# Kernel tuning notes

Hardware: AMD Instinct MI355X
Metric: run time of the kernel (lower is better)

Reference implementation:

```python
import jax, jax.numpy as jnp
import numpy as np

N_NODES = 40000
IN_CH, HID_CH, OUT_CH = 128, 128, 64
N_EDGES = 640000
N_LABEL = 200000


def gcn_conv(x, edge_index, W, b):
    """PyG-style GCNConv: x' = D^{-1/2}(A+I)D^{-1/2} (x W) + b."""
    n = x.shape[0]
    loops = jnp.arange(n, dtype=edge_index.dtype)
    src = jnp.concatenate([edge_index[0], loops])  # [E+N]
    dst = jnp.concatenate([edge_index[1], loops])  # [E+N]
    deg = jax.ops.segment_sum(jnp.ones_like(dst, dtype=x.dtype), dst, num_segments=n)
    dinv = jnp.where(deg > 0, jax.lax.rsqrt(deg), 0.0)
    norm = dinv[src] * dinv[dst]                   # [E+N]
    h = x @ W                                      # [n, out]
    msg = h[src] * norm[:, None]                   # gather + scale
    agg = jax.ops.segment_sum(msg, dst, num_segments=n)
    return agg + b


def setup_inputs() -> dict:
    key = jax.random.key(0)
    k = jax.random.split(key, 8)
    x = jax.random.normal(k[0], (N_NODES, IN_CH), dtype=jnp.float32)
    edge_index = jax.random.randint(k[1], (2, N_EDGES), 0, N_NODES, dtype=jnp.int64)
    edge_label_index = jax.random.randint(k[2], (2, N_LABEL), 0, N_NODES, dtype=jnp.int64)
    s1 = 1.0 / np.sqrt(IN_CH)
    s2 = 1.0 / np.sqrt(HID_CH)
    W1 = jax.random.uniform(k[3], (IN_CH, HID_CH), jnp.float32, -s1, s1)
    b1 = jnp.zeros((HID_CH,), jnp.float32)
    W2 = jax.random.uniform(k[4], (HID_CH, OUT_CH), jnp.float32, -s2, s2)
    b2 = jnp.zeros((OUT_CH,), jnp.float32)
    return {"x": x, "edge_index": edge_index, "edge_label_index": edge_label_index,
            "W1": W1, "b1": b1, "W2": W2, "b2": b2}


def reference(x, edge_index, edge_label_index, W1, b1, W2, b2):
    # encode: conv1 -> relu -> conv2
    h = jax.nn.relu(gcn_conv(x, edge_index, W1, b1))
    z = gcn_conv(h, edge_index, W2, b2)            # [N, OUT_CH]
    # decode: dot-product score per candidate edge
    logits = jnp.sum(z[edge_label_index[0]] * z[edge_label_index[1]], axis=-1)
    return logits
```

## Files before the change

kernel.cpp:

```cpp
#include <hip/hip_runtime.h>
#include <hip/hip_bf16.h>

constexpr int IN_CH  = 128;
constexpr int HID_CH = 128;
constexpr int OUT_CH = 64;
constexpr int SCAN_CHUNK = 1024;

typedef __attribute__((ext_vector_type(8))) short bf16x8;
typedef __attribute__((ext_vector_type(4))) float f32x4;


__device__ inline unsigned short f2bf(float f) {
  __hip_bfloat16 h = __float2bfloat16(f);
  return *reinterpret_cast<unsigned short*>(&h);
}
__device__ inline unsigned pack_bf16x2(float lo, float hi) {
  return (unsigned)f2bf(lo) | ((unsigned)f2bf(hi) << 16);
}
__device__ inline float bf_lo(unsigned u) { return __uint_as_float(u << 16); }
__device__ inline float bf_hi(unsigned u) { return __uint_as_float(u & 0xffff0000u); }


__global__ __launch_bounds__(256) void k_zero(int* __restrict__ a, int n) {
  int i = (blockIdx.x * 256 + threadIdx.x) * 4;
  if (i + 3 < n) *(int4*)&a[i] = make_int4(0, 0, 0, 0);
  else for (int j = 0; j < 4 && i + j < n; ++j) a[i + j] = 0;
}


__global__ void k_count(const int* __restrict__ dst, int* __restrict__ cnt,
                        int* __restrict__ ord, int E) {
  int e = (blockIdx.x * blockDim.x + threadIdx.x) * 4;
  if (e + 3 < E) {
    int4 v = *(const int4*)&dst[e];
    int4 o;
    o.x = atomicAdd(&cnt[v.x], 1);
    o.y = atomicAdd(&cnt[v.y], 1);
    o.z = atomicAdd(&cnt[v.z], 1);
    o.w = atomicAdd(&cnt[v.w], 1);
    *(int4*)&ord[e] = o;
  } else {
    for (int j = 0; j < 4 && e + j < E; ++j) ord[e + j] = atomicAdd(&cnt[dst[e + j]], 1);
  }
}

__global__ __launch_bounds__(256) void k_scan_part(const int* __restrict__ cnt,
                                                   int* __restrict__ bsum,
                                                   float* __restrict__ dinv, int N) {
  int t = threadIdx.x;
  int base = blockIdx.x * SCAN_CHUNK + t * 4;
  int s = 0;
  if (base + 3 < N) {
    int4 v = *(const int4*)&cnt[base];
    s = v.x + v.y + v.z + v.w;
    float4 d;
    d.x = rsqrtf((float)v.x + 1.0f);
    d.y = rsqrtf((float)v.y + 1.0f);
    d.z = rsqrtf((float)v.z + 1.0f);
    d.w = rsqrtf((float)v.w + 1.0f);
    *(float4*)&dinv[base] = d;
  } else {
    for (int j = 0; j < 4; ++j)
      if (base + j < N) {
        int c = cnt[base + j];
        s += c;
        dinv[base + j] = rsqrtf((float)c + 1.0f);
      }
  }
  __shared__ int red[256];
  red[t] = s; __syncthreads();
  for (int off = 128; off; off >>= 1) {
    if (t < off) red[t] += red[t + off];
    __syncthreads();
  }
  if (t == 0) bsum[blockIdx.x] = red[0];
}

__global__ __launch_bounds__(256) void k_scan_fill(const int* __restrict__ cnt,
                                                   const int* __restrict__ bsum,
                                                   int* __restrict__ rowptr, int N, int E) {
  int t = threadIdx.x;
  int boff = 0;
  for (int i = 0; i < blockIdx.x; ++i) boff += bsum[i];
  int base = blockIdx.x * SCAN_CHUNK + t * 4;
  int v[4] = {0, 0, 0, 0};
  if (base + 3 < N) {
    int4 q = *(const int4*)&cnt[base];
    v[0] = q.x; v[1] = q.y; v[2] = q.z; v[3] = q.w;
  } else {
    for (int j = 0; j < 4; ++j) if (base + j < N) v[j] = cnt[base + j];
  }
  int mysum = v[0] + v[1] + v[2] + v[3];
  __shared__ int s[256];
  s[t] = mysum; __syncthreads();
  for (int off = 1; off < 256; off <<= 1) {
    int add = (t >= off) ? s[t - off] : 0;
    __syncthreads();
    s[t] += add;
    __syncthreads();
  }
  int run = boff + s[t] - mysum;
  for (int j = 0; j < 4; ++j) {
    if (base + j < N) rowptr[base + j] = run;
    run += v[j];
  }
  if (blockIdx.x == 0 && t == 0) rowptr[N] = E;
}

__global__ void k_fill(const int* __restrict__ src, const int* __restrict__ dst,
                       const int* __restrict__ ord, const int* __restrict__ rowptr,
                       int* __restrict__ col, int E) {
  int e0 = (blockIdx.x * blockDim.x + threadIdx.x) * 4;
  if (e0 >= E) return;
  if (e0 + 3 < E) {
    int4 sv = *(const int4*)&src[e0];
    int4 dv = *(const int4*)&dst[e0];
    int4 ov = *(const int4*)&ord[e0];
    col[rowptr[dv.x] + ov.x] = sv.x;
    col[rowptr[dv.y] + ov.y] = sv.y;
    col[rowptr[dv.z] + ov.z] = sv.z;
    col[rowptr[dv.w] + ov.w] = sv.w;
  } else {
    for (int j = 0; j < 4 && e0 + j < E; ++j)
      col[rowptr[dst[e0 + j]] + ord[e0 + j]] = src[e0 + j];
  }
}


template <int OUT, bool A_BF16>
__global__ __launch_bounds__(256) void k_gemm(const void* __restrict__ Xv,
                                              const float* __restrict__ W,
                                              const float* __restrict__ dinv,
                                              unsigned short* __restrict__ Y, int N) {
  constexpr int KD = 128;
  __shared__ unsigned short Wt[OUT * KD];
  int t = threadIdx.x;
  for (int i = t * 4; i < KD * OUT; i += 1024) {
    int k = i / OUT, c = i % OUT;
    float4 w4 = *(const float4*)&W[i];
    float wa[4] = {w4.x, w4.y, w4.z, w4.w};
#pragma unroll
    for (int j = 0; j < 4; ++j) {
      int colj = c + j;
      int byte = colj * (KD * 2) + k * 2;
      byte ^= ((colj & 7) << 4);
      *(unsigned short*)((char*)Wt + byte) = f2bf(wa[j]);
    }
  }
  __syncthreads();

  int w = t >> 6, l = t & 63;
  int lr = l & 15, kg = (l >> 4) * 8;
  int r = blockIdx.x * 64 + w * 16 + lr;
  bool valid = r < N;

  f32x4 acc[OUT / 16];
#pragma unroll
  for (int n = 0; n < OUT / 16; ++n) acc[n] = f32x4{0.f, 0.f, 0.f, 0.f};

#pragma unroll
  for (int kb = 0; kb < KD / 32; ++kb) {
    bf16x8 a = bf16x8{0, 0, 0, 0, 0, 0, 0, 0};
    if (valid) {
      if (A_BF16) {
        a = *(const bf16x8*)((const unsigned short*)Xv + (size_t)r * KD + kb * 32 + kg);
      } else {
        const float* xrow = (const float*)Xv + (size_t)r * KD + kb * 32 + kg;
        float4 x0 = *(const float4*)xrow;
        float4 x1 = *(const float4*)(xrow + 4);
        a[0] = (short)f2bf(x0.x); a[1] = (short)f2bf(x0.y);
        a[2] = (short)f2bf(x0.z); a[3] = (short)f2bf(x0.w);
        a[4] = (short)f2bf(x1.x); a[5] = (short)f2bf(x1.y);
        a[6] = (short)f2bf(x1.z); a[7] = (short)f2bf(x1.w);
      }
    }
#pragma unroll
    for (int n = 0; n < OUT / 16; ++n) {
      int col = n * 16 + lr;
      int byte = col * (KD * 2) + (kb * 32 + kg) * 2;
      byte ^= ((col & 7) << 4);
      bf16x8 b = *(const bf16x8*)((const char*)Wt + byte);
      acc[n] = __builtin_amdgcn_mfma_f32_16x16x32_bf16(a, b, acc[n], 0, 0, 0);
    }
  }

  int orow = blockIdx.x * 64 + w * 16 + (l >> 4) * 4;
  float dn[4];
#pragma unroll
  for (int i = 0; i < 4; ++i) dn[i] = (orow + i < N) ? dinv[orow + i] : 0.f;
#pragma unroll
  for (int i = 0; i < 4; ++i) {
    if (orow + i >= N) continue;
#pragma unroll
    for (int n = 0; n < OUT / 16; ++n)
      Y[(size_t)(orow + i) * OUT + n * 16 + lr] = f2bf(acc[n][i] * dn[i]);
  }
}


__global__ __launch_bounds__(256) void k_agg128(const unsigned* __restrict__ HS,
                                                const int* __restrict__ rowptr,
                                                const int* __restrict__ col,
                                                const float* __restrict__ dinv,
                                                const float* __restrict__ bias,
                                                unsigned* __restrict__ Outb, int N) {
  int n = blockIdx.x * 4 + (threadIdx.x >> 6);
  if (n >= N) return;
  int l = threadIdx.x & 63;
  float dn = dinv[n];
  unsigned u0 = HS[(size_t)n * 64 + l];
  float ax = bf_lo(u0), ay = bf_hi(u0);
  int p = rowptr[n], pend = rowptr[n + 1];
  for (; p + 8 <= pend; p += 8) {
    int s[8]; unsigned g[8];
#pragma unroll
    for (int j = 0; j < 8; ++j) s[j] = col[p + j];
#pragma unroll
    for (int j = 0; j < 8; ++j) g[j] = HS[(size_t)s[j] * 64 + l];
#pragma unroll
    for (int j = 0; j < 8; ++j) { ax += bf_lo(g[j]); ay += bf_hi(g[j]); }
  }
  for (; p < pend; ++p) {
    unsigned g = HS[(size_t)col[p] * 64 + l];
    ax += bf_lo(g); ay += bf_hi(g);
  }
  float2 b2 = ((const float2*)bias)[l];
  Outb[(size_t)n * 64 + l] =
      pack_bf16x2(fmaxf(dn * ax + b2.x, 0.f), fmaxf(dn * ay + b2.y, 0.f));
}


__global__ __launch_bounds__(256) void k_agg64(const unsigned* __restrict__ HS,
                                               const int* __restrict__ rowptr,
                                               const int* __restrict__ col,
                                               const float* __restrict__ dinv,
                                               const float* __restrict__ bias,
                                               unsigned* __restrict__ Zu, int N) {
  int n = blockIdx.x * 8 + (threadIdx.x >> 5);
  if (n >= N) return;
  int g = threadIdx.x & 31;
  float dn = dinv[n];
  unsigned u0 = HS[(size_t)n * 32 + g];
  float ax = bf_lo(u0), ay = bf_hi(u0);
  int p = rowptr[n], pend = rowptr[n + 1];
  for (; p + 8 <= pend; p += 8) {
    int s[8]; unsigned q[8];
#pragma unroll
    for (int j = 0; j < 8; ++j) s[j] = col[p + j];
#pragma unroll
    for (int j = 0; j < 8; ++j) q[j] = HS[(size_t)s[j] * 32 + g];
#pragma unroll
    for (int j = 0; j < 8; ++j) { ax += bf_lo(q[j]); ay += bf_hi(q[j]); }
  }
  for (; p < pend; ++p) {
    unsigned q = HS[(size_t)col[p] * 32 + g];
    ax += bf_lo(q); ay += bf_hi(q);
  }
  float2 b2 = ((const float2*)bias)[g];
  Zu[(size_t)n * 32 + g] = pack_bf16x2(dn * ax + b2.x, dn * ay + b2.y);
}


__global__ __launch_bounds__(256) void k_decode(const uint4* __restrict__ Z,
                                                const int* __restrict__ ia,
                                                const int* __restrict__ ib,
                                                float* __restrict__ out, int L) {
  int t = blockIdx.x * 256 + threadIdx.x;
  int i = t >> 3;
  if (i >= L) return;
  int e = t & 7;
  int a = ia[i], b = ib[i];
  uint4 za = Z[(size_t)a * 8 + e];
  uint4 zb = Z[(size_t)b * 8 + e];
  float p = bf_lo(za.x) * bf_lo(zb.x) + bf_hi(za.x) * bf_hi(zb.x)
          + bf_lo(za.y) * bf_lo(zb.y) + bf_hi(za.y) * bf_hi(zb.y)
          + bf_lo(za.z) * bf_lo(zb.z) + bf_hi(za.z) * bf_hi(zb.z)
          + bf_lo(za.w) * bf_lo(zb.w) + bf_hi(za.w) * bf_hi(zb.w);
  p += __shfl_xor(p, 1);
  p += __shfl_xor(p, 2);
  p += __shfl_xor(p, 4);
  if (e == 0) out[i] = p;
}

extern "C" void kernel_launch(void* const* d_in, const int* in_sizes, int n_in,
                              void* d_out, int out_size, void* d_ws, size_t ws_size,
                              hipStream_t stream) {
  const float* x   = (const float*)d_in[0];
  const int*   ei  = (const int*)d_in[1];
  const int*   eli = (const int*)d_in[2];
  const float* W1  = (const float*)d_in[3];
  const float* b1  = (const float*)d_in[4];
  const float* W2  = (const float*)d_in[5];
  const float* b2  = (const float*)d_in[6];
  float* logits = (float*)d_out;

  int N = in_sizes[0] / IN_CH;
  int E = in_sizes[1] / 2;
  int L = in_sizes[2] / 2;
  const int* src = ei;
  const int* dst = ei + E;
  const int* la  = eli;
  const int* lb  = eli + L;

  char* ws = (char*)d_ws;
  size_t off = 0;
  auto alloc = [&](size_t bytes) {
    void* p = ws + off;
    off = (off + bytes + 255) & ~(size_t)255;
    return p;
  };
  int*      cnt    = (int*)alloc((size_t)N * 4);
  int*      rowptr = (int*)alloc((size_t)(N + 1) * 4);
  float*    dinv   = (float*)alloc((size_t)N * 4);
  int*      col    = (int*)alloc((size_t)E * 4);
  int*      ord    = (int*)alloc((size_t)E * 4);
  unsigned short* hs  = (unsigned short*)alloc((size_t)N * HID_CH * 2);
  unsigned* hrb    = (unsigned*)alloc((size_t)N * HID_CH * 2);
  unsigned short* h2s = (unsigned short*)alloc((size_t)N * OUT_CH * 2);
  unsigned* zu     = (unsigned*)alloc((size_t)N * OUT_CH * 2);
  int*      bsum   = (int*)alloc(256 * 4);

  const int TB = 256;
  int nscan = (N + SCAN_CHUNK - 1) / SCAN_CHUNK;
  k_zero<<<(N / 4 + TB - 1) / TB, TB, 0, stream>>>(cnt, N);
  k_count<<<(E / 4 + TB - 1) / TB, TB, 0, stream>>>(dst, cnt, ord, E);
  k_scan_part<<<nscan, 256, 0, stream>>>(cnt, bsum, dinv, N);
  k_scan_fill<<<nscan, 256, 0, stream>>>(cnt, bsum, rowptr, N, E);
  k_fill <<<(E / 4 + TB - 1) / TB, TB, 0, stream>>>(src, dst, ord, rowptr, col, E);

  k_gemm<HID_CH, false><<<(N + 63) / 64, 256, 0, stream>>>(x, W1, dinv, hs, N);
  k_agg128<<<(N + 3) / 4, 256, 0, stream>>>((const unsigned*)hs, rowptr, col, dinv, b1, hrb, N);

  k_gemm<OUT_CH, true><<<(N + 63) / 64, 256, 0, stream>>>(hrb, W2, dinv, h2s, N);
  k_agg64<<<(N + 7) / 8, 256, 0, stream>>>((const unsigned*)h2s, rowptr, col, dinv, b2, zu, N);

  k_decode<<<((size_t)L * 8 + 255) / 256, 256, 0, stream>>>((const uint4*)zu, la, lb, logits, L);
}
```

Baseline: 135.3 us.

## Split feature tables into 32-channel planes mapped to XCDs for L2 locality

Stores hidden and output features as planar 32-channel slices (pass-major) instead of row-major, and assigns each slice to a fixed subset of XCDs via block-id decoding so each XCD's L2 only caches its slice during gathers. Aggregation now uses 16-lane groups with four edge streams per node reduced by shuffles, replacing separate agg128/agg64 kernels with one template. Decode is split across two planes with atomicAdd into a zeroed output, which adds a zeroing step and atomics and relies on the block-to-XCD round-robin assumption.

After: 213.2 us. 57.6% more time.

```diff
diff --git a/kernel.cpp b/kernel.cpp
--- a/kernel.cpp
+++ b/kernel.cpp
@@ -21,10 +21,13 @@
 __device__ inline float bf_hi(unsigned u) { return __uint_as_float(u & 0xffff0000u); }
 
 
-__global__ __launch_bounds__(256) void k_zero(int* __restrict__ a, int n) {
+__global__ __launch_bounds__(256) void k_zero(int* __restrict__ a, int na,
+                                              float* __restrict__ b, int nb) {
   int i = (blockIdx.x * 256 + threadIdx.x) * 4;
-  if (i + 3 < n) *(int4*)&a[i] = make_int4(0, 0, 0, 0);
-  else for (int j = 0; j < 4 && i + j < n; ++j) a[i + j] = 0;
+  if (i + 3 < na) *(int4*)&a[i] = make_int4(0, 0, 0, 0);
+  else for (int j = 0; j < 4 && i + j < na; ++j) a[i + j] = 0;
+  if (i + 3 < nb) *(float4*)&b[i] = make_float4(0.f, 0.f, 0.f, 0.f);
+  else for (int j = 0; j < 4 && i + j < nb; ++j) b[i + j] = 0.f;
 }
 
 
@@ -163,7 +166,7 @@
     bf16x8 a = bf16x8{0, 0, 0, 0, 0, 0, 0, 0};
     if (valid) {
       if (A_BF16) {
-        a = *(const bf16x8*)((const unsigned short*)Xv + (size_t)r * KD + kb * 32 + kg);
+        a = *(const bf16x8*)((const unsigned short*)Xv + ((size_t)kb * N + r) * 32 + kg);
       } else {
         const float* xrow = (const float*)Xv + (size_t)r * KD + kb * 32 + kg;
         float4 x0 = *(const float4*)xrow;
@@ -193,93 +196,85 @@
     if (orow + i >= N) continue;
 #pragma unroll
     for (int n = 0; n < OUT / 16; ++n)
-      Y[(size_t)(orow + i) * OUT + n * 16 + lr] = f2bf(acc[n][i] * dn[i]);
-  }
-}
-
-
-__global__ __launch_bounds__(256) void k_agg128(const unsigned* __restrict__ HS,
-                                                const int* __restrict__ rowptr,
-                                                const int* __restrict__ col,
-                                                const float* __restrict__ dinv,
-                                                const float* __restrict__ bias,
-                                                unsigned* __restrict__ Outb, int N) {
-  int n = blockIdx.x * 4 + (threadIdx.x >> 6);
+      Y[((size_t)(n >> 1) * N + (orow + i)) * 32 + (n & 1) * 16 + lr] =
+          f2bf(acc[n][i] * dn[i]);
+  }
+}
+
+
+template <int NPASS, bool RELU>
+__global__ __launch_bounds__(256) void k_agg(const unsigned* __restrict__ T,
+                                             const int* __restrict__ rowptr,
+                                             const int* __restrict__ col,
+                                             const float* __restrict__ dinv,
+                                             const float* __restrict__ bias,
+                                             unsigned* __restrict__ Out, int N) {
+  constexpr int SUBS = 8 / NPASS;
+  int bid = blockIdx.x;
+  int xcd = bid & 7, chunk = bid >> 3;
+  int pass = xcd / SUBS, sub = xcd % SUBS;
+  int w = threadIdx.x >> 6, l = threadIdx.x & 63;
+  int n = (chunk * SUBS + sub) * 4 + w;
   if (n >= N) return;
-  int l = threadIdx.x & 63;
+  int grp = l >> 4, cp = l & 15;
+  const unsigned* Tp = T + (size_t)pass * N * 16;
   float dn = dinv[n];
-  unsigned u0 = HS[(size_t)n * 64 + l];
-  float ax = bf_lo(u0), ay = bf_hi(u0);
-  int p = rowptr[n], pend = rowptr[n + 1];
-  for (; p + 8 <= pend; p += 8) {
-    int s[8]; unsigned g[8];
-#pragma unroll
-    for (int j = 0; j < 8; ++j) s[j] = col[p + j];
-#pragma unroll
-    for (int j = 0; j < 8; ++j) g[j] = HS[(size_t)s[j] * 64 + l];
-#pragma unroll
-    for (int j = 0; j < 8; ++j) { ax += bf_lo(g[j]); ay += bf_hi(g[j]); }
-  }
-  for (; p < pend; ++p) {
-    unsigned g = HS[(size_t)col[p] * 64 + l];
-    ax += bf_lo(g); ay += bf_hi(g);
-  }
-  float2 b2 = ((const float2*)bias)[l];
-  Outb[(size_t)n * 64 + l] =
-      pack_bf16x2(fmaxf(dn * ax + b2.x, 0.f), fmaxf(dn * ay + b2.y, 0.f));
-}
-
-
-__global__ __launch_bounds__(256) void k_agg64(const unsigned* __restrict__ HS,
-                                               const int* __restrict__ rowptr,
-                                               const int* __restrict__ col,
-                                               const float* __restrict__ dinv,
-                                               const float* __restrict__ bias,
-                                               unsigned* __restrict__ Zu, int N) {
-  int n = blockIdx.x * 8 + (threadIdx.x >> 5);
-  if (n >= N) return;
-  int g = threadIdx.x & 31;
-  float dn = dinv[n];
-  unsigned u0 = HS[(size_t)n * 32 + g];
-  float ax = bf_lo(u0), ay = bf_hi(u0);
-  int p = rowptr[n], pend = rowptr[n + 1];
-  for (; p + 8 <= pend; p += 8) {
-    int s[8]; unsigned q[8];
-#pragma unroll
-    for (int j = 0; j < 8; ++j) s[j] = col[p + j];
-#pragma unroll
-    for (int j = 0; j < 8; ++j) q[j] = HS[(size_t)s[j] * 32 + g];
-#pragma unroll
-    for (int j = 0; j < 8; ++j) { ax += bf_lo(q[j]); ay += bf_hi(q[j]); }
-  }
-  for (; p < pend; ++p) {
-    unsigned q = HS[(size_t)col[p] * 32 + g];
-    ax += bf_lo(q); ay += bf_hi(q);
-  }
-  float2 b2 = ((const float2*)bias)[g];
-  Zu[(size_t)n * 32 + g] = pack_bf16x2(dn * ax + b2.x, dn * ay + b2.y);
-}
-
-
-__global__ __launch_bounds__(256) void k_decode(const uint4* __restrict__ Z,
+  float ax = 0.f, ay = 0.f;
+  if (grp == 0) {
+    unsigned u0 = Tp[(size_t)n * 16 + cp];
+    ax = bf_lo(u0); ay = bf_hi(u0);
+  }
+  int pend = rowptr[n + 1];
+  int e = rowptr[n] + grp;
+  for (; e + 12 < pend; e += 16) {
+    int c0 = __builtin_nontemporal_load(&col[e]);
+    int c1 = __builtin_nontemporal_load(&col[e + 4]);
+    int c2 = __builtin_nontemporal_load(&col[e + 8]);
+    int c3 = __builtin_nontemporal_load(&col[e + 12]);
+    unsigned u0 = Tp[(size_t)c0 * 16 + cp];
+    unsigned u1 = Tp[(size_t)c1 * 16 + cp];
+    unsigned u2 = Tp[(size_t)c2 * 16 + cp];
+    unsigned u3 = Tp[(size_t)c3 * 16 + cp];
+    ax += bf_lo(u0) + bf_lo(u1) + bf_lo(u2) + bf_lo(u3);
+    ay += bf_hi(u0) + bf_hi(u1) + bf_hi(u2) + bf_hi(u3);
+  }
+  for (; e < pend; e += 4) {
+    int c = __builtin_nontemporal_load(&col[e]);
+    unsigned u = Tp[(size_t)c * 16 + cp];
+    ax += bf_lo(u); ay += bf_hi(u);
+  }
+  ax += __shfl_xor(ax, 16); ax += __shfl_xor(ax, 32);
+  ay += __shfl_xor(ay, 16); ay += __shfl_xor(ay, 32);
+  if (grp == 0) {
+    float2 b2 = ((const float2*)(bias + pass * 32))[cp];
+    float vx = dn * ax + b2.x, vy = dn * ay + b2.y;
+    if (RELU) { vx = fmaxf(vx, 0.f); vy = fmaxf(vy, 0.f); }
+    Out[(size_t)pass * N * 16 + (size_t)n * 16 + cp] = pack_bf16x2(vx, vy);
+  }
+}
+
+
+__global__ __launch_bounds__(256) void k_decode(const unsigned* __restrict__ Z,
                                                 const int* __restrict__ ia,
                                                 const int* __restrict__ ib,
-                                                float* __restrict__ out, int L) {
-  int t = blockIdx.x * 256 + threadIdx.x;
-  int i = t >> 3;
+                                                float* __restrict__ out, int N, int L) {
+  int bid = blockIdx.x;
+  int xcd = bid & 7, chunk = bid >> 3;
+  int pass = xcd >> 2, sub = xcd & 3;
+  int t = threadIdx.x;
+  int i = (chunk * 4 + sub) * 16 + (t >> 4);
   if (i >= L) return;
-  int e = t & 7;
+  int e = t & 15;
   int a = ia[i], b = ib[i];
-  uint4 za = Z[(size_t)a * 8 + e];
-  uint4 zb = Z[(size_t)b * 8 + e];
-  float p = bf_lo(za.x) * bf_lo(zb.x) + bf_hi(za.x) * bf_hi(zb.x)
-          + bf_lo(za.y) * bf_lo(zb.y) + bf_hi(za.y) * bf_hi(zb.y)
-          + bf_lo(za.z) * bf_lo(zb.z) + bf_hi(za.z) * bf_hi(zb.z)
-          + bf_lo(za.w) * bf_lo(zb.w) + bf_hi(za.w) * bf_hi(zb.w);
+  const unsigned* Zp = Z + (size_t)pass * N * 16;
+  unsigned za = Zp[(size_t)a * 16 + e];
+  unsigned zb = Zp[(size_t)b * 16 + e];
+  float p = bf_lo(za) * bf_lo(zb) + bf_hi(za) * bf_hi(zb);
   p += __shfl_xor(p, 1);
   p += __shfl_xor(p, 2);
   p += __shfl_xor(p, 4);
-  if (e == 0) out[i] = p;
+  p += __shfl_xor(p, 8);
+  if (e == 0) atomicAdd(&out[i], p);
 }
 
 extern "C" void kernel_launch(void* const* d_in, const int* in_sizes, int n_in,
@@ -314,25 +309,29 @@
   float*    dinv   = (float*)alloc((size_t)N * 4);
   int*      col    = (int*)alloc((size_t)E * 4);
   int*      ord    = (int*)alloc((size_t)E * 4);
-  unsigned short* hs  = (unsigned short*)alloc((size_t)N * HID_CH * 2);
-  unsigned* hrb    = (unsigned*)alloc((size_t)N * HID_CH * 2);
-  unsigned short* h2s = (unsigned short*)alloc((size_t)N * OUT_CH * 2);
-  unsigned* zu     = (unsigned*)alloc((size_t)N * OUT_CH * 2);
+  unsigned short* hsp  = (unsigned short*)alloc((size_t)N * HID_CH * 2);
+  unsigned short* hrbp = (unsigned short*)alloc((size_t)N * HID_CH * 2);
+  unsigned short* h2sp = (unsigned short*)alloc((size_t)N * OUT_CH * 2);
+  unsigned short* zup  = (unsigned short*)alloc((size_t)N * OUT_CH * 2);
   int*      bsum   = (int*)alloc(256 * 4);
 
   const int TB = 256;
   int nscan = (N + SCAN_CHUNK - 1) / SCAN_CHUNK;
-  k_zero<<<(N / 4 + TB - 1) / TB, TB, 0, stream>>>(cnt, N);
+  int nzero = max(N, L);
+  k_zero<<<(nzero / 4 + TB - 1) / TB, TB, 0, stream>>>(cnt, N, logits, L);
   k_count<<<(E / 4 + TB - 1) / TB, TB, 0, stream>>>(dst, cnt, ord, E);
   k_scan_part<<<nscan, 256, 0, stream>>>(cnt, bsum, dinv, N);
   k_scan_fill<<<nscan, 256, 0, stream>>>(cnt, bsum, rowptr, N, E);
   k_fill <<<(E / 4 + TB - 1) / TB, TB, 0, stream>>>(src, dst, ord, rowptr, col, E);
 
-  k_gemm<HID_CH, false><<<(N + 63) / 64, 256, 0, stream>>>(x, W1, dinv, hs, N);
-  k_agg128<<<(N + 3) / 4, 256, 0, stream>>>((const unsigned*)hs, rowptr, col, dinv, b1, hrb, N);
-
-  k_gemm<OUT_CH, true><<<(N + 63) / 64, 256, 0, stream>>>(hrb, W2, dinv, h2s, N);
-  k_agg64<<<(N + 7) / 8, 256, 0, stream>>>((const unsigned*)h2s, rowptr, col, dinv, b2, zu, N);
-
-  k_decode<<<((size_t)L * 8 + 255) / 256, 256, 0, stream>>>((const uint4*)zu, la, lb, logits, L);
-}
+  k_gemm<HID_CH, false><<<(N + 63) / 64, 256, 0, stream>>>(x, W1, dinv, hsp, N);
+  k_agg<4, true><<<((N + 7) / 8) * 8, 256, 0, stream>>>(
+      (const unsigned*)hsp, rowptr, col, dinv, b1, (unsigned*)hrbp, N);
+
+  k_gemm<OUT_CH, true><<<(N + 63) / 64, 256, 0, stream>>>(hrbp, W2, dinv, h2sp, N);
+  k_agg<2, false><<<((N + 15) / 16) * 8, 256, 0, stream>>>(
+      (const unsigned*)h2sp, rowptr, col, dinv, b2, (unsigned*)zup, N);
+
+  k_decode<<<((L + 63) / 64) * 8, 256, 0, stream>>>(
+      (const unsigned*)zup, la, lb, logits, N, L);
+}
```

## Split feature tables into two column halves with XCD-aware aggregation scheduling

Applied to the files above, without the earlier changes.

The GEMM outputs and aggregation outputs now use a two-plane layout, each plane holding half the feature columns for all nodes. The aggregation kernel is unified into a template and maps block IDs so blocks on XCDs 0-3 handle the first half and XCDs 4-7 the second. The aim is to shrink each XCD's gather working set so it stays in its L2. It also adds nontemporal loads of the column indices and a 4-edge tail step, at the cost of more complex indexing in the GEMM, aggregation and decode kernels.

After: 144.4 us. +6.7%, slower.

```diff
diff --git a/kernel.cpp b/kernel.cpp
--- a/kernel.cpp
+++ b/kernel.cpp
@@ -133,6 +133,7 @@
                                               const float* __restrict__ dinv,
                                               unsigned short* __restrict__ Y, int N) {
   constexpr int KD = 128;
+  constexpr int NCG = OUT / 32;
   __shared__ unsigned short Wt[OUT * KD];
   int t = threadIdx.x;
   for (int i = t * 4; i < KD * OUT; i += 1024) {
@@ -163,7 +164,8 @@
     bf16x8 a = bf16x8{0, 0, 0, 0, 0, 0, 0, 0};
     if (valid) {
       if (A_BF16) {
-        a = *(const bf16x8*)((const unsigned short*)Xv + (size_t)r * KD + kb * 32 + kg);
+        a = *(const bf16x8*)((const unsigned short*)Xv +
+                             ((size_t)(kb >> 1) * N + r) * 64 + (kb & 1) * 32 + kg);
       } else {
         const float* xrow = (const float*)Xv + (size_t)r * KD + kb * 32 + kg;
         float4 x0 = *(const float4*)xrow;
@@ -193,85 +195,75 @@
     if (orow + i >= N) continue;
 #pragma unroll
     for (int n = 0; n < OUT / 16; ++n)
-      Y[(size_t)(orow + i) * OUT + n * 16 + lr] = f2bf(acc[n][i] * dn[i]);
-  }
-}
-
-
-__global__ __launch_bounds__(256) void k_agg128(const unsigned* __restrict__ HS,
-                                                const int* __restrict__ rowptr,
-                                                const int* __restrict__ col,
-                                                const float* __restrict__ dinv,
-                                                const float* __restrict__ bias,
-                                                unsigned* __restrict__ Outb, int N) {
-  int n = blockIdx.x * 4 + (threadIdx.x >> 6);
+      Y[((size_t)(n / NCG) * N + (orow + i)) * (OUT / 2) + (n % NCG) * 16 + lr] =
+          f2bf(acc[n][i] * dn[i]);
+  }
+}
+
+
+template <int CPU, bool RELU>
+__global__ __launch_bounds__(256) void k_agg(const unsigned* __restrict__ T,
+                                             const int* __restrict__ rowptr,
+                                             const int* __restrict__ col,
+                                             const float* __restrict__ dinv,
+                                             const float* __restrict__ bias,
+                                             unsigned* __restrict__ Out, int N) {
+  constexpr int NPW = 64 / CPU;
+  constexpr int NPB = 4 * NPW;
+  int bid = blockIdx.x;
+  int xcd = bid & 7, chunk = bid >> 3;
+  int pass = xcd >> 2, sub = xcd & 3;
+  int w = threadIdx.x >> 6, l = threadIdx.x & 63;
+  int n = (chunk * 4 + sub) * NPB + w * NPW + l / CPU;
   if (n >= N) return;
-  int l = threadIdx.x & 63;
+  int cp = l % CPU;
+  const unsigned* Tp = T + (size_t)pass * N * CPU;
   float dn = dinv[n];
-  unsigned u0 = HS[(size_t)n * 64 + l];
+  unsigned u0 = Tp[(size_t)n * CPU + cp];
   float ax = bf_lo(u0), ay = bf_hi(u0);
   int p = rowptr[n], pend = rowptr[n + 1];
   for (; p + 8 <= pend; p += 8) {
     int s[8]; unsigned g[8];
 #pragma unroll
-    for (int j = 0; j < 8; ++j) s[j] = col[p + j];
-#pragma unroll
-    for (int j = 0; j < 8; ++j) g[j] = HS[(size_t)s[j] * 64 + l];
+    for (int j = 0; j < 8; ++j) s[j] = __builtin_nontemporal_load(&col[p + j]);
+#pragma unroll
+    for (int j = 0; j < 8; ++j) g[j] = Tp[(size_t)s[j] * CPU + cp];
 #pragma unroll
     for (int j = 0; j < 8; ++j) { ax += bf_lo(g[j]); ay += bf_hi(g[j]); }
   }
+  if (p + 4 <= pend) {
+    int s[4]; unsigned g[4];
+#pragma unroll
+    for (int j = 0; j < 4; ++j) s[j] = __builtin_nontemporal_load(&col[p + j]);
+#pragma unroll
+    for (int j = 0; j < 4; ++j) g[j] = Tp[(size_t)s[j] * CPU + cp];
+#pragma unroll
+    for (int j = 0; j < 4; ++j) { ax += bf_lo(g[j]); ay += bf_hi(g[j]); }
+    p += 4;
+  }
   for (; p < pend; ++p) {
-    unsigned g = HS[(size_t)col[p] * 64 + l];
+    unsigned g = Tp[(size_t)__builtin_nontemporal_load(&col[p]) * CPU + cp];
     ax += bf_lo(g); ay += bf_hi(g);
   }
-  float2 b2 = ((const float2*)bias)[l];
-  Outb[(size_t)n * 64 + l] =
-      pack_bf16x2(fmaxf(dn * ax + b2.x, 0.f), fmaxf(dn * ay + b2.y, 0.f));
-}
-
-
-__global__ __launch_bounds__(256) void k_agg64(const unsigned* __restrict__ HS,
-                                               const int* __restrict__ rowptr,
-                                               const int* __restrict__ col,
-                                               const float* __restrict__ dinv,
-                                               const float* __restrict__ bias,
-                                               unsigned* __restrict__ Zu, int N) {
-  int n = blockIdx.x * 8 + (threadIdx.x >> 5);
-  if (n >= N) return;
-  int g = threadIdx.x & 31;
-  float dn = dinv[n];
-  unsigned u0 = HS[(size_t)n * 32 + g];
-  float ax = bf_lo(u0), ay = bf_hi(u0);
-  int p = rowptr[n], pend = rowptr[n + 1];
-  for (; p + 8 <= pend; p += 8) {
-    int s[8]; unsigned q[8];
-#pragma unroll
-    for (int j = 0; j < 8; ++j) s[j] = col[p + j];
-#pragma unroll
-    for (int j = 0; j < 8; ++j) q[j] = HS[(size_t)s[j] * 32 + g];
-#pragma unroll
-    for (int j = 0; j < 8; ++j) { ax += bf_lo(q[j]); ay += bf_hi(q[j]); }
-  }
-  for (; p < pend; ++p) {
-    unsigned q = HS[(size_t)col[p] * 32 + g];
-    ax += bf_lo(q); ay += bf_hi(q);
-  }
-  float2 b2 = ((const float2*)bias)[g];
-  Zu[(size_t)n * 32 + g] = pack_bf16x2(dn * ax + b2.x, dn * ay + b2.y);
-}
-
-
-__global__ __launch_bounds__(256) void k_decode(const uint4* __restrict__ Z,
+  float2 b2 = ((const float2*)bias)[pass * CPU + cp];
+  float vx = dn * ax + b2.x, vy = dn * ay + b2.y;
+  if (RELU) { vx = fmaxf(vx, 0.f); vy = fmaxf(vy, 0.f); }
+  Out[(size_t)pass * N * CPU + (size_t)n * CPU + cp] = pack_bf16x2(vx, vy);
+}
+
+
+__global__ __launch_bounds__(256) void k_decode(const unsigned* __restrict__ Z,
                                                 const int* __restrict__ ia,
                                                 const int* __restrict__ ib,
-                                                float* __restrict__ out, int L) {
+                                                float* __restrict__ out, int N, int L) {
   int t = blockIdx.x * 256 + threadIdx.x;
   int i = t >> 3;
   if (i >= L) return;
   int e = t & 7;
   int a = ia[i], b = ib[i];
-  uint4 za = Z[(size_t)a * 8 + e];
-  uint4 zb = Z[(size_t)b * 8 + e];
+  size_t base = (size_t)(e >> 2) * N * 16 + (size_t)(e & 3) * 4;
+  uint4 za = *(const uint4*)&Z[base + (size_t)a * 16];
+  uint4 zb = *(const uint4*)&Z[base + (size_t)b * 16];
   float p = bf_lo(za.x) * bf_lo(zb.x) + bf_hi(za.x) * bf_hi(zb.x)
           + bf_lo(za.y) * bf_lo(zb.y) + bf_hi(za.y) * bf_hi(zb.y)
           + bf_lo(za.z) * bf_lo(zb.z) + bf_hi(za.z) * bf_hi(zb.z)
@@ -314,10 +306,10 @@
   float*    dinv   = (float*)alloc((size_t)N * 4);
   int*      col    = (int*)alloc((size_t)E * 4);
   int*      ord    = (int*)alloc((size_t)E * 4);
-  unsigned short* hs  = (unsigned short*)alloc((size_t)N * HID_CH * 2);
-  unsigned* hrb    = (unsigned*)alloc((size_t)N * HID_CH * 2);
-  unsigned short* h2s = (unsigned short*)alloc((size_t)N * OUT_CH * 2);
-  unsigned* zu     = (unsigned*)alloc((size_t)N * OUT_CH * 2);
+  unsigned short* hsp  = (unsigned short*)alloc((size_t)N * HID_CH * 2);
+  unsigned short* hrbp = (unsigned short*)alloc((size_t)N * HID_CH * 2);
+  unsigned short* h2sp = (unsigned short*)alloc((size_t)N * OUT_CH * 2);
+  unsigned short* zup  = (unsigned short*)alloc((size_t)N * OUT_CH * 2);
   int*      bsum   = (int*)alloc(256 * 4);
 
   const int TB = 256;
@@ -328,11 +320,20 @@
   k_scan_fill<<<nscan, 256, 0, stream>>>(cnt, bsum, rowptr, N, E);
   k_fill <<<(E / 4 + TB - 1) / TB, TB, 0, stream>>>(src, dst, ord, rowptr, col, E);
 
-  k_gemm<HID_CH, false><<<(N + 63) / 64, 256, 0, stream>>>(x, W1, dinv, hs, N);
-  k_agg128<<<(N + 3) / 4, 256, 0, stream>>>((const unsigned*)hs, rowptr, col, dinv, b1, hrb, N);
-
-  k_gemm<OUT_CH, true><<<(N + 63) / 64, 256, 0, stream>>>(hrb, W2, dinv, h2s, N);
-  k_agg64<<<(N + 7) / 8, 256, 0, stream>>>((const unsigned*)h2s, rowptr, col, dinv, b2, zu, N);
-
-  k_decode<<<((size_t)L * 8 + 255) / 256, 256, 0, stream>>>((const uint4*)zu, la, lb, logits, L);
-}
+  k_gemm<HID_CH, false><<<(N + 63) / 64, 256, 0, stream>>>(x, W1, dinv, hsp, N);
+  {
+    int nchunk = (N + 8 * 4 - 1) / (8 * 4);
+    k_agg<32, true><<<nchunk * 8, 256, 0, stream>>>(
+        (const unsigned*)hsp, rowptr, col, dinv, b1, (unsigned*)hrbp, N);
+  }
+
+  k_gemm<OUT_CH, true><<<(N + 63) / 64, 256, 0, stream>>>(hrbp, W2, dinv, h2sp, N);
+  {
+    int nchunk = (N + 16 * 4 - 1) / (16 * 4);
+    k_agg<16, false><<<nchunk * 8, 256, 0, stream>>>(
+        (const unsigned*)h2sp, rowptr, col, dinv, b2, (unsigned*)zup, N);
+  }
+
+  k_decode<<<((size_t)L * 8 + 255) / 256, 256, 0, stream>>>(
+      (const unsigned*)zup, la, lb, logits, N, L);
+}
```

## Merge scan kernels, fuse CSR fill with first GEMM, widen aggregation loads

Applied to the files above, without the earlier changes.

Replaces the two-pass prefix scan with a single kernel that chains block partials through flags and spin-waits on earlier blocks, and zeroes those flags in the existing zero kernel. The CSR column fill and the first GEMM now share one launch, split by block index. Both aggregation kernels move to 8-byte loads per lane with half as many lanes per node, add a 4-wide tail step, and read column indices with nontemporal loads. The goal is fewer launches and less per-lane gather overhead. The spin-wait relies on all 40 scan blocks being resident at once.

After: 129.2 us, median of 2. 4.5% less time.

```diff
diff --git a/kernel.cpp b/kernel.cpp
--- a/kernel.cpp
+++ b/kernel.cpp
@@ -21,10 +21,13 @@
 __device__ inline float bf_hi(unsigned u) { return __uint_as_float(u & 0xffff0000u); }
 
 
-__global__ __launch_bounds__(256) void k_zero(int* __restrict__ a, int n) {
+__global__ __launch_bounds__(256) void k_zero(int* __restrict__ a, int na,
+                                              int* __restrict__ b, int nb) {
   int i = (blockIdx.x * 256 + threadIdx.x) * 4;
-  if (i + 3 < n) *(int4*)&a[i] = make_int4(0, 0, 0, 0);
-  else for (int j = 0; j < 4 && i + j < n; ++j) a[i + j] = 0;
+  if (i + 3 < na) *(int4*)&a[i] = make_int4(0, 0, 0, 0);
+  else for (int j = 0; j < 4 && i + j < na; ++j) a[i + j] = 0;
+  if (i + 3 < nb) *(int4*)&b[i] = make_int4(0, 0, 0, 0);
+  else for (int j = 0; j < 4 && i + j < nb; ++j) b[i + j] = 0;
 }
 
 
@@ -44,51 +47,30 @@
   }
 }
 
-__global__ __launch_bounds__(256) void k_scan_part(const int* __restrict__ cnt,
-                                                   int* __restrict__ bsum,
-                                                   float* __restrict__ dinv, int N) {
-  int t = threadIdx.x;
-  int base = blockIdx.x * SCAN_CHUNK + t * 4;
-  int s = 0;
+__global__ __launch_bounds__(256) void k_scan_lb(const int* __restrict__ cnt,
+                                                 int* __restrict__ rowptr,
+                                                 float* __restrict__ dinv,
+                                                 int* __restrict__ flags,
+                                                 int* __restrict__ partial,
+                                                 int N, int E) {
+  int t = threadIdx.x, bid = blockIdx.x;
+  int base = bid * SCAN_CHUNK + t * 4;
+  int v[4] = {0, 0, 0, 0};
   if (base + 3 < N) {
-    int4 v = *(const int4*)&cnt[base];
-    s = v.x + v.y + v.z + v.w;
+    int4 q = *(const int4*)&cnt[base];
+    v[0] = q.x; v[1] = q.y; v[2] = q.z; v[3] = q.w;
     float4 d;
-    d.x = rsqrtf((float)v.x + 1.0f);
-    d.y = rsqrtf((float)v.y + 1.0f);
-    d.z = rsqrtf((float)v.z + 1.0f);
-    d.w = rsqrtf((float)v.w + 1.0f);
+    d.x = rsqrtf((float)v[0] + 1.0f);
+    d.y = rsqrtf((float)v[1] + 1.0f);
+    d.z = rsqrtf((float)v[2] + 1.0f);
+    d.w = rsqrtf((float)v[3] + 1.0f);
     *(float4*)&dinv[base] = d;
   } else {
     for (int j = 0; j < 4; ++j)
       if (base + j < N) {
-        int c = cnt[base + j];
-        s += c;
-        dinv[base + j] = rsqrtf((float)c + 1.0f);
+        v[j] = cnt[base + j];
+        dinv[base + j] = rsqrtf((float)v[j] + 1.0f);
       }
-  }
-  __shared__ int red[256];
-  red[t] = s; __syncthreads();
-  for (int off = 128; off; off >>= 1) {
-    if (t < off) red[t] += red[t + off];
-    __syncthreads();
-  }
-  if (t == 0) bsum[blockIdx.x] = red[0];
-}
-
-__global__ __launch_bounds__(256) void k_scan_fill(const int* __restrict__ cnt,
-                                                   const int* __restrict__ bsum,
-                                                   int* __restrict__ rowptr, int N, int E) {
-  int t = threadIdx.x;
-  int boff = 0;
-  for (int i = 0; i < blockIdx.x; ++i) boff += bsum[i];
-  int base = blockIdx.x * SCAN_CHUNK + t * 4;
-  int v[4] = {0, 0, 0, 0};
-  if (base + 3 < N) {
-    int4 q = *(const int4*)&cnt[base];
-    v[0] = q.x; v[1] = q.y; v[2] = q.z; v[3] = q.w;
-  } else {
-    for (int j = 0; j < 4; ++j) if (base + j < N) v[j] = cnt[base + j];
   }
   int mysum = v[0] + v[1] + v[2] + v[3];
   __shared__ int s[256];
@@ -99,39 +81,38 @@
     s[t] += add;
     __syncthreads();
   }
-  int run = boff + s[t] - mysum;
+  if (t == 255) {
+    partial[bid] = s[255];
+    __threadfence();
+    atomicExch(&flags[bid], 1);
+  }
+  int pv = 0;
+  if (t < bid) {
+    while (atomicAdd(&flags[t], 0) == 0) {}
+    __threadfence();
+    pv = atomicAdd(&partial[t], 0);
+  }
+  __shared__ int boff_s;
+  if (t < 64) {
+#pragma unroll
+    for (int off = 32; off; off >>= 1) pv += __shfl_down(pv, off);
+    if (t == 0) boff_s = pv;
+  }
+  __syncthreads();
+  int run = boff_s + s[t] - mysum;
   for (int j = 0; j < 4; ++j) {
     if (base + j < N) rowptr[base + j] = run;
     run += v[j];
   }
-  if (blockIdx.x == 0 && t == 0) rowptr[N] = E;
-}
-
-__global__ void k_fill(const int* __restrict__ src, const int* __restrict__ dst,
-                       const int* __restrict__ ord, const int* __restrict__ rowptr,
-                       int* __restrict__ col, int E) {
-  int e0 = (blockIdx.x * blockDim.x + threadIdx.x) * 4;
-  if (e0 >= E) return;
-  if (e0 + 3 < E) {
-    int4 sv = *(const int4*)&src[e0];
-    int4 dv = *(const int4*)&dst[e0];
-    int4 ov = *(const int4*)&ord[e0];
-    col[rowptr[dv.x] + ov.x] = sv.x;
-    col[rowptr[dv.y] + ov.y] = sv.y;
-    col[rowptr[dv.z] + ov.z] = sv.z;
-    col[rowptr[dv.w] + ov.w] = sv.w;
-  } else {
-    for (int j = 0; j < 4 && e0 + j < E; ++j)
-      col[rowptr[dst[e0 + j]] + ord[e0 + j]] = src[e0 + j];
-  }
+  if (bid == 0 && t == 0) rowptr[N] = E;
 }
 
 
 template <int OUT, bool A_BF16>
-__global__ __launch_bounds__(256) void k_gemm(const void* __restrict__ Xv,
-                                              const float* __restrict__ W,
-                                              const float* __restrict__ dinv,
-                                              unsigned short* __restrict__ Y, int N) {
+__device__ inline void gemm_body(int gb, const void* __restrict__ Xv,
+                                 const float* __restrict__ W,
+                                 const float* __restrict__ dinv,
+                                 unsigned short* __restrict__ Y, int N) {
   constexpr int KD = 128;
   __shared__ unsigned short Wt[OUT * KD];
   int t = threadIdx.x;
@@ -151,7 +132,7 @@
 
   int w = t >> 6, l = t & 63;
   int lr = l & 15, kg = (l >> 4) * 8;
-  int r = blockIdx.x * 64 + w * 16 + lr;
+  int r = gb * 64 + w * 16 + lr;
   bool valid = r < N;
 
   f32x4 acc[OUT / 16];
@@ -184,7 +165,7 @@
     }
   }
 
-  int orow = blockIdx.x * 64 + w * 16 + (l >> 4) * 4;
+  int orow = gb * 64 + w * 16 + (l >> 4) * 4;
   float dn[4];
 #pragma unroll
   for (int i = 0; i < 4; ++i) dn[i] = (orow + i < N) ? dinv[orow + i] : 0.f;
@@ -197,67 +178,142 @@
   }
 }
 
-
-__global__ __launch_bounds__(256) void k_agg128(const unsigned* __restrict__ HS,
+template <int OUT, bool A_BF16>
+__global__ __launch_bounds__(256) void k_fill_gemm(const int* __restrict__ src,
+                                                   const int* __restrict__ dst,
+                                                   const int* __restrict__ ord,
+                                                   const int* __restrict__ rowptr,
+                                                   int* __restrict__ col, int E, int nfill,
+                                                   const void* __restrict__ Xv,
+                                                   const float* __restrict__ W,
+                                                   const float* __restrict__ dinv,
+                                                   unsigned short* __restrict__ Y, int N) {
+  if ((int)blockIdx.x < nfill) {
+    int e0 = (blockIdx.x * 256 + threadIdx.x) * 4;
+    if (e0 >= E) return;
+    if (e0 + 3 < E) {
+      int4 sv = *(const int4*)&src[e0];
+      int4 dv = *(const int4*)&dst[e0];
+      int4 ov = *(const int4*)&ord[e0];
+      col[rowptr[dv.x] + ov.x] = sv.x;
+      col[rowptr[dv.y] + ov.y] = sv.y;
+      col[rowptr[dv.z] + ov.z] = sv.z;
+      col[rowptr[dv.w] + ov.w] = sv.w;
+    } else {
+      for (int j = 0; j < 4 && e0 + j < E; ++j)
+        col[rowptr[dst[e0 + j]] + ord[e0 + j]] = src[e0 + j];
+    }
+    return;
+  }
+  gemm_body<OUT, A_BF16>((int)blockIdx.x - nfill, Xv, W, dinv, Y, N);
+}
+
+template <int OUT, bool A_BF16>
+__global__ __launch_bounds__(256) void k_gemm(const void* __restrict__ Xv,
+                                              const float* __restrict__ W,
+                                              const float* __restrict__ dinv,
+                                              unsigned short* __restrict__ Y, int N) {
+  gemm_body<OUT, A_BF16>((int)blockIdx.x, Xv, W, dinv, Y, N);
+}
+
+
+__global__ __launch_bounds__(256) void k_agg128(const uint2* __restrict__ HS,
                                                 const int* __restrict__ rowptr,
                                                 const int* __restrict__ col,
                                                 const float* __restrict__ dinv,
                                                 const float* __restrict__ bias,
-                                                unsigned* __restrict__ Outb, int N) {
-  int n = blockIdx.x * 4 + (threadIdx.x >> 6);
+                                                uint2* __restrict__ Outb, int N) {
+  int n = blockIdx.x * 8 + (threadIdx.x >> 5);
   if (n >= N) return;
-  int l = threadIdx.x & 63;
+  int c = threadIdx.x & 31;
   float dn = dinv[n];
-  unsigned u0 = HS[(size_t)n * 64 + l];
-  float ax = bf_lo(u0), ay = bf_hi(u0);
+  uint2 u0 = HS[(size_t)n * 32 + c];
+  float ax = bf_lo(u0.x), ay = bf_hi(u0.x), az = bf_lo(u0.y), aw = bf_hi(u0.y);
   int p = rowptr[n], pend = rowptr[n + 1];
   for (; p + 8 <= pend; p += 8) {
-    int s[8]; unsigned g[8];
-#pragma unroll
-    for (int j = 0; j < 8; ++j) s[j] = col[p + j];
-#pragma unroll
-    for (int j = 0; j < 8; ++j) g[j] = HS[(size_t)s[j] * 64 + l];
-#pragma unroll
-    for (int j = 0; j < 8; ++j) { ax += bf_lo(g[j]); ay += bf_hi(g[j]); }
+    int s[8]; uint2 g[8];
+#pragma unroll
+    for (int j = 0; j < 8; ++j) s[j] = __builtin_nontemporal_load(&col[p + j]);
+#pragma unroll
+    for (int j = 0; j < 8; ++j) g[j] = HS[(size_t)s[j] * 32 + c];
+#pragma unroll
+    for (int j = 0; j < 8; ++j) {
+      ax += bf_lo(g[j].x); ay += bf_hi(g[j].x);
+      az += bf_lo(g[j].y); aw += bf_hi(g[j].y);
+    }
+  }
+  if (p + 4 <= pend) {
+    int s[4]; uint2 g[4];
+#pragma unroll
+    for (int j = 0; j < 4; ++j) s[j] = __builtin_nontemporal_load(&col[p + j]);
+#pragma unroll
+    for (int j = 0; j < 4; ++j) g[j] = HS[(size_t)s[j] * 32 + c];
+#pragma unroll
+    for (int j = 0; j < 4; ++j) {
+      ax += bf_lo(g[j].x); ay += bf_hi(g[j].x);
+      az += bf_lo(g[j].y); aw += bf_hi(g[j].y);
+    }
+    p += 4;
   }
   for (; p < pend; ++p) {
-    unsigned g = HS[(size_t)col[p] * 64 + l];
-    ax += bf_lo(g); ay += bf_hi(g);
-  }
-  float2 b2 = ((const float2*)bias)[l];
-  Outb[(size_t)n * 64 + l] =
-      pack_bf16x2(fmaxf(dn * ax + b2.x, 0.f), fmaxf(dn * ay + b2.y, 0.f));
-}
-
-
-__global__ __launch_bounds__(256) void k_agg64(const unsigned* __restrict__ HS,
+    uint2 g = HS[(size_t)__builtin_nontemporal_load(&col[p]) * 32 + c];
+    ax += bf_lo(g.x); ay += bf_hi(g.x); az += bf_lo(g.y); aw += bf_hi(g.y);
+  }
+  float4 b4 = ((const float4*)bias)[c];
+  uint2 ov;
+  ov.x = pack_bf16x2(fmaxf(dn * ax + b4.x, 0.f), fmaxf(dn * ay + b4.y, 0.f));
+  ov.y = pack_bf16x2(fmaxf(dn * az + b4.z, 0.f), fmaxf(dn * aw + b4.w, 0.f));
+  Outb[(size_t)n * 32 + c] = ov;
+}
+
+
+__global__ __launch_bounds__(256) void k_agg64(const uint2* __restrict__ HS,
                                                const int* __restrict__ rowptr,
                                                const int* __restrict__ col,
                                                const float* __restrict__ dinv,
                                                const float* __restrict__ bias,
-                                               unsigned* __restrict__ Zu, int N) {
-  int n = blockIdx.x * 8 + (threadIdx.x >> 5);
+                                               uint2* __restrict__ Zu, int N) {
+  int n = blockIdx.x * 16 + (threadIdx.x >> 4);
   if (n >= N) return;
-  int g = threadIdx.x & 31;
+  int c = threadIdx.x & 15;
   float dn = dinv[n];
-  unsigned u0 = HS[(size_t)n * 32 + g];
-  float ax = bf_lo(u0), ay = bf_hi(u0);
+  uint2 u0 = HS[(size_t)n * 16 + c];
+  float ax = bf_lo(u0.x), ay = bf_hi(u0.x), az = bf_lo(u0.y), aw = bf_hi(u0.y);
   int p = rowptr[n], pend = rowptr[n + 1];
   for (; p + 8 <= pend; p += 8) {
-    int s[8]; unsigned q[8];
-#pragma unroll
-    for (int j = 0; j < 8; ++j) s[j] = col[p + j];
-#pragma unroll
-    for (int j = 0; j < 8; ++j) q[j] = HS[(size_t)s[j] * 32 + g];
-#pragma unroll
-    for (int j = 0; j < 8; ++j) { ax += bf_lo(q[j]); ay += bf_hi(q[j]); }
+    int s[8]; uint2 g[8];
+#pragma unroll
+    for (int j = 0; j < 8; ++j) s[j] = __builtin_nontemporal_load(&col[p + j]);
+#pragma unroll
+    for (int j = 0; j < 8; ++j) g[j] = HS[(size_t)s[j] * 16 + c];
+#pragma unroll
+    for (int j = 0; j < 8; ++j) {
+      ax += bf_lo(g[j].x); ay += bf_hi(g[j].x);
+      az += bf_lo(g[j].y); aw += bf_hi(g[j].y);
+    }
+  }
+  if (p + 4 <= pend) {
+    int s[4]; uint2 g[4];
+#pragma unroll
+    for (int j = 0; j < 4; ++j) s[j] = __builtin_nontemporal_load(&col[p + j]);
+#pragma unroll
+    for (int j = 0; j < 4; ++j) g[j] = HS[(size_t)s[j] * 16 + c];
+#pragma unroll
+    for (int j = 0; j < 4; ++j) {
+      ax += bf_lo(g[j].x); ay += bf_hi(g[j].x);
+      az += bf_lo(g[j].y); aw += bf_hi(g[j].y);
+    }
+    p += 4;
   }
   for (; p < pend; ++p) {
-    unsigned q = HS[(size_t)col[p] * 32 + g];
-    ax += bf_lo(q); ay += bf_hi(q);
-  }
-  float2 b2 = ((const float2*)bias)[g];
-  Zu[(size_t)n * 32 + g] = pack_bf16x2(dn * ax + b2.x, dn * ay + b2.y);
+    uint2 g = HS[(size_t)__builtin_nontemporal_load(&col[p]) * 16 + c];
+    ax += bf_lo(g.x); ay += bf_hi(g.x); az += bf_lo(g.y); aw += bf_hi(g.y);
+  }
+  float4 b4 = ((const float4*)bias)[c];
+  uint2 ov;
+  ov.x = pack_bf16x2(dn * ax + b4.x, dn * ay + b4.y);
+  ov.y = pack_bf16x2(dn * az + b4.z, dn * aw + b4.w);
+  Zu[(size_t)n * 16 + c] = ov;
 }
 
 
@@ -315,24 +371,30 @@
   int*      col    = (int*)alloc((size_t)E * 4);
   int*      ord    = (int*)alloc((size_t)E * 4);
   unsigned short* hs  = (unsigned short*)alloc((size_t)N * HID_CH * 2);
-  unsigned* hrb    = (unsigned*)alloc((size_t)N * HID_CH * 2);
+  unsigned short* hrb = (unsigned short*)alloc((size_t)N * HID_CH * 2);
   unsigned short* h2s = (unsigned short*)alloc((size_t)N * OUT_CH * 2);
-  unsigned* zu     = (unsigned*)alloc((size_t)N * OUT_CH * 2);
-  int*      bsum   = (int*)alloc(256 * 4);
+  unsigned short* zu  = (unsigned short*)alloc((size_t)N * OUT_CH * 2);
+  int*      flags  = (int*)alloc(64 * 4);
+  int*      partial= (int*)alloc(64 * 4);
 
   const int TB = 256;
   int nscan = (N + SCAN_CHUNK - 1) / SCAN_CHUNK;
-  k_zero<<<(N / 4 + TB - 1) / TB, TB, 0, stream>>>(cnt, N);
+  int nfill = (E / 4 + TB - 1) / TB;
+  int ngemm = (N + 63) / 64;
+  k_zero<<<(N / 4 + TB - 1) / TB, TB, 0, stream>>>(cnt, N, flags, 64);
   k_count<<<(E / 4 + TB - 1) / TB, TB, 0, stream>>>(dst, cnt, ord, E);
-  k_scan_part<<<nscan, 256, 0, stream>>>(cnt, bsum, dinv, N);
-  k_scan_fill<<<nscan, 256, 0, stream>>>(cnt, bsum, rowptr, N, E);
-  k_fill <<<(E / 4 + TB - 1) / TB, TB, 0, stream>>>(src, dst, ord, rowptr, col, E);
-
-  k_gemm<HID_CH, false><<<(N + 63) / 64, 256, 0, stream>>>(x, W1, dinv, hs, N);
-  k_agg128<<<(N + 3) / 4, 256, 0, stream>>>((const unsigned*)hs, rowptr, col, dinv, b1, hrb, N);
-
-  k_gemm<OUT_CH, true><<<(N + 63) / 64, 256, 0, stream>>>(hrb, W2, dinv, h2s, N);
-  k_agg64<<<(N + 7) / 8, 256, 0, stream>>>((const unsigned*)h2s, rowptr, col, dinv, b2, zu, N);
-
-  k_decode<<<((size_t)L * 8 + 255) / 256, 256, 0, stream>>>((const uint4*)zu, la, lb, logits, L);
-}
+  k_scan_lb<<<nscan, 256, 0, stream>>>(cnt, rowptr, dinv, flags, partial, N, E);
+
+  k_fill_gemm<HID_CH, false><<<nfill + ngemm, 256, 0, stream>>>(
+      src, dst, ord, rowptr, col, E, nfill, x, W1, dinv, hs, N);
+
+  k_agg128<<<(N + 7) / 8, 256, 0, stream>>>(
+      (const uint2*)hs, rowptr, col, dinv, b1, (uint2*)hrb, N);
+
+  k_gemm<OUT_CH, true><<<ngemm, 256, 0, stream>>>(hrb, W2, dinv, h2s, N);
+  k_agg64<<<(N + 15) / 16, 256, 0, stream>>>(
+      (const uint2*)h2s, rowptr, col, dinv, b2, (uint2*)zu, N);
+
+  k_decode<<<((size_t)L * 8 + 255) / 256, 256, 0, stream>>>(
+      (const uint4*)zu, la, lb, logits, L);
+}
```
